# Performance work log

Measured on AMD Instinct MI355X. Metric: run time of the kernel, lower is better.

## Reference

```python
import jax, jax.numpy as jnp
import numpy as np

B = 1024        # batch_size (len(c_ids))
D = 128         # dim_proto
N_AFE_A = 2     # len(AFE_a_ids_selected) == l_a
N_AFE_R = 2     # len(AFE_r_ids_selected) == l_r
S = 16          # sum(n_nbs_per_hop) = 10 + 6
A = 4096        # num_atoms (active codebook rows)
L = N_AFE_A + N_AFE_R * S  # 34


def _normalize(x, eps=1e-12):
    # torch F.normalize(dim=-1): x / max(||x||_2, eps)
    n = jnp.linalg.norm(x, axis=-1, keepdims=True)
    return x / jnp.maximum(n, eps)


def setup_inputs() -> dict:
    key = jax.random.key(0)
    k1, k2, k3 = jax.random.split(key, 3)
    embeddings = jax.random.normal(k1, (B, L, D), dtype=jnp.float32)
    atoms = jax.random.uniform(k2, (A, D), dtype=jnp.float32, minval=0.0, maxval=0.5)
    W_att = jax.random.normal(k3, ((N_AFE_A + N_AFE_R * S) * D, N_AFE_R * S + N_AFE_A), dtype=jnp.float32) * 0.02
    b_att = jnp.zeros((N_AFE_R * S + N_AFE_A,), dtype=jnp.float32)
    return {"embeddings": embeddings, "atoms": atoms, "W_att": W_att, "b_att": b_att}


def reference(embeddings, atoms, W_att, b_att):
    atoms_n = _normalize(atoms)  # F.normalize(self.atoms[0:num_atoms], dim=-1), [A, D]

    # --- attribute emb sets: embeddings[:, i, :] for i in range(n_AFE_a) ---
    attr = embeddings[:, :N_AFE_A, :]                                 # [B, la, D]
    soft_a = jnp.einsum('bld,ad->bla', attr, atoms_n)                 # similarity vs codebook
    hard_a = (soft_a == soft_a.max(axis=-1, keepdims=True)).astype(jnp.float32)
    assoc_a = jnp.einsum('bla,ad->bld', hard_a, atoms)                # one-hot @ atoms (lookup)

    # --- relational emb sets: chunks of size S, flattened to [B*S, D] in torch ---
    rel = embeddings[:, N_AFE_A:, :].reshape(B, N_AFE_R, S, D)
    soft_r = jnp.einsum('brsd,ad->brsa', rel, atoms_n)
    hard_r = (soft_r == soft_r.max(axis=-1, keepdims=True)).astype(jnp.float32)
    assoc_r = jnp.einsum('brsa,ad->brsd', hard_r, atoms).reshape(B, N_AFE_R * S, D)

    # per-row L2 normalize each associated prototype, then concat along slot dim
    assoc = jnp.concatenate([_normalize(assoc_a), _normalize(assoc_r)], axis=1)  # [B, la+lr*S, D]

    # attention aggregation: Linear over flattened slots, then bmm
    a = assoc.reshape(B, (N_AFE_A + N_AFE_R * S) * D)
    att = a @ W_att + b_att                                           # [B, la+lr*S]
    obj_embs = _normalize(jnp.einsum('bl,bld->bd', att, assoc))       # [B, D]
    return obj_embs
```

## Files before the change

kernel.cpp:

```cpp
#include <hip/hip_runtime.h>
#include <math.h>

#define BB 1024
#define LL 34
#define DD 128
#define AA 4096
#define NROWS (BB * LL)
#define RTILES (NROWS / 16)
#define ATILES (AA / 16)
#define NSPLIT 8
#define TPS (ATILES / NSPLIT)
#define TAU 2.5e-3f
#define SCOREBLKS ((RTILES / 16) * NSPLIT)
#define GTABBLKS (LL * 32)

typedef _Float16 f16;
typedef _Float16 f16x8 __attribute__((ext_vector_type(8)));
typedef float f32x4  __attribute__((ext_vector_type(4)));

#define OFF_EMBA   0u
#define OFF_ATOMB  8912896u
#define OFF_WFRAG  9961472u
#define OFF_G      10379264u
#define OFF_PQ     30433280u
#define OFF_INVN64 34889728u
#define OFF_INVNF  34922496u

__global__ __launch_bounds__(256) void k_prep(const float* __restrict__ emb,
                                              const float* __restrict__ atoms,
                                              const float* __restrict__ W,
                                              double* __restrict__ invn64,
                                              float* __restrict__ invnF,
                                              f16x8* __restrict__ embA,
                                              f16x8* __restrict__ atomB,
                                              f16x8* __restrict__ wfrag) {
    __shared__ __align__(16) float stbuf[4608];
    __shared__ double part[16][17];
    const int bid = blockIdx.x;
    const int tid = threadIdx.x;

    if (bid < RTILES + ATILES) {
        const bool isAtom = (bid >= RTILES);
        const int tile = isAtom ? bid - RTILES : bid;
        const float* src = (isAtom ? atoms : emb) + (size_t)tile * 2048;
        float4* st4 = (float4*)stbuf;
        for (int i = tid; i < 512; i += 256) {
            int row = i >> 5, c4 = i & 31;
            st4[row * 33 + c4] = ((const float4*)src)[i];
        }
        __syncthreads();

        const int ks = tid >> 6, l = tid & 63;
        const int m = l & 15, koff4 = ((l >> 4) << 1) + (ks << 3);
        float4 f0 = st4[m * 33 + koff4];
        float4 f1 = st4[m * 33 + koff4 + 1];
        float xs[8] = {f0.x, f0.y, f0.z, f0.w, f1.x, f1.y, f1.z, f1.w};

        if (!isAtom) {
            f16x8 h;
            #pragma unroll
            for (int j = 0; j < 8; j++) h[j] = (f16)xs[j];
            embA[(size_t)(tile * 4 + ks) * 64 + l] = h;
        } else {
            double ssq = 0.0;
            #pragma unroll
            for (int j = 0; j < 8; j++) ssq += (double)xs[j] * xs[j];
            part[m][ks * 4 + (l >> 4)] = ssq;
            __syncthreads();
            double tot = 0.0;
            #pragma unroll
            for (int q = 0; q < 16; q++) tot += part[m][q];
            double n = sqrt(tot);
            if (n < 1e-12) n = 1e-12;
            double inv = 1.0 / n;
            float invf = (float)inv;
            f16x8 h;
            #pragma unroll
            for (int j = 0; j < 8; j++) h[j] = (f16)(xs[j] * invf);
            if (ks == 0 && (l >> 4) == 0) {
                invn64[tile * 16 + m] = inv;
                invnF[tile * 16 + m] = invf;
            }
            atomB[(size_t)(tile * 4 + ks) * 64 + l] = h;
        }
    } else {
        const int l = bid - RTILES - ATILES;
        const float* wsrc = W + (size_t)l * 128 * LL;
        for (int i = tid; i < 128 * LL; i += 256) {
            int row = i / LL, j = i - row * LL;
            stbuf[row * 35 + j] = wsrc[i];
        }
        __syncthreads();
        for (int s = tid; s < 768; s += 256) {
            int lane = s & 63, ksnt = s >> 6;
            int ks = ksnt & 3, nt = ksnt >> 2;
            int j = nt * 16 + (lane & 15);
            int kb = ks * 32 + ((lane >> 4) << 3);
            f16x8 h;
            if (j < LL) {
                #pragma unroll
                for (int jj = 0; jj < 8; jj++) h[jj] = (f16)stbuf[(kb + jj) * 35 + j];
            } else {
                #pragma unroll
                for (int jj = 0; jj < 8; jj++) h[jj] = (f16)0.f;
            }
            wfrag[(size_t)((l * 3 + nt) * 4 + ks) * 64 + lane] = h;
        }
    }
}

__global__ __launch_bounds__(256, 3) void k_score(const f16x8* __restrict__ embA,
                                                  const char* __restrict__ atomB,
                                                  const f16x8* __restrict__ wfrag,
                                                  float* __restrict__ G,
                                                  float4* __restrict__ pq) {
    const int tid = threadIdx.x;
    const int w = tid >> 6, l = tid & 63;

    if (blockIdx.x >= SCOREBLKS) {
        __shared__ __align__(16) float gs[128 * 36];
        const int gb = blockIdx.x - SCOREBLKS;
        const int ll = gb >> 5, ab = gb & 31;

        f16x8 bw[3][4];
        #pragma unroll
        for (int nt = 0; nt < 3; nt++)
            #pragma unroll
            for (int ks = 0; ks < 4; ks++)
                bw[nt][ks] = wfrag[(size_t)((ll * 3 + nt) * 4 + ks) * 64 + l];

        const int col = l & 15, rq = (l >> 4) * 4;
        #pragma unroll
        for (int t = 0; t < 2; t++) {
            int atile = ab * 8 + w * 2 + t;
            f16x8 ah[4];
            #pragma unroll
            for (int ks = 0; ks < 4; ks++)
                ah[ks] = *(const f16x8*)(atomB + ((size_t)(atile * 4 + ks) * 64 + l) * 16);
            f32x4 acc[3];
            #pragma unroll
            for (int nt = 0; nt < 3; nt++) acc[nt] = (f32x4){0.f, 0.f, 0.f, 0.f};
            #pragma unroll
            for (int ks = 0; ks < 4; ks++)
                #pragma unroll
                for (int nt = 0; nt < 3; nt++)
                    acc[nt] = __builtin_amdgcn_mfma_f32_16x16x32_f16(ah[ks], bw[nt][ks], acc[nt], 0, 0, 0);
            int aloc0 = (w * 2 + t) * 16 + rq;
            #pragma unroll
            for (int nt = 0; nt < 3; nt++) {
                int j = nt * 16 + col;
                if (j < LL) {
                    #pragma unroll
                    for (int r = 0; r < 4; r++)
                        gs[(aloc0 + r) * 36 + j] = acc[nt][r];
                }
            }
        }
        __syncthreads();
        float* Gl = G + ((size_t)ll * 4096 + ab * 128) * 36;
        for (int i = tid; i < 128 * 36; i += 256) Gl[i] = gs[i];
        return;
    }

    const int sp = blockIdx.x / 136, rb = blockIdx.x - sp * 136;
    const int rt0 = rb * 16 + w * 4;

    f16x8 a[4][4];
    #pragma unroll
    for (int f = 0; f < 4; f++)
        #pragma unroll
        for (int ks = 0; ks < 4; ks++)
            a[f][ks] = embA[(size_t)((rt0 + f) * 4 + ks) * 64 + l];

    float v1[16], v2[16];
    #pragma unroll
    for (int s = 0; s < 16; s++) { v1[s] = -3e38f; v2[s] = -3e38f; }

    const f16x8* bbase = (const f16x8*)(atomB) + (size_t)sp * TPS * 256;

    #define LOADT(BUF, T)                                            \
        {                                                            \
            _Pragma("unroll")                                        \
            for (int ks = 0; ks < 4; ks++)                           \
                BUF[ks] = bbase[(size_t)(T) * 256 + ks * 64 + l];    \
        }

    #define COMP(BUF, T)                                                          \
        {                                                                         \
            f32x4 acc[4];                                                         \
            _Pragma("unroll")                                                     \
            for (int f = 0; f < 4; f++) acc[f] = (f32x4){0.f, 0.f, 0.f, 0.f};     \
            _Pragma("unroll")                                                     \
            for (int ks = 0; ks < 4; ks++)                                        \
                _Pragma("unroll")                                                 \
                for (int f = 0; f < 4; f++)                                       \
                    acc[f] = __builtin_amdgcn_mfma_f32_16x16x32_f16(a[f][ks], BUF[ks], acc[f], 0, 0, 0); \
            const unsigned tl = (unsigned)(T);                                    \
            _Pragma("unroll")                                                     \
            for (int f = 0; f < 4; f++)                                           \
                _Pragma("unroll")                                                 \
                for (int r = 0; r < 4; r++) {                                     \
                    int s = f * 4 + r;                                            \
                    float xq = __uint_as_float((__float_as_uint(acc[f][r]) & 0xFFFFFFE0u) | tl); \
                    v2[s] = __builtin_amdgcn_fmed3f(xq, v1[s], v2[s]);            \
                    v1[s] = fmaxf(v1[s], xq);                                     \
                }                                                                 \
        }

    f16x8 c0[4], c1[4];
    LOADT(c0, 0);
    for (int t = 0; t < TPS; t += 2) {
        LOADT(c1, t + 1);
        COMP(c0, t);
        if (t + 2 < TPS) LOADT(c0, t + 2);
        COMP(c1, t + 1);
    }
    #undef LOADT
    #undef COMP

    float vv1[16], vv2[16];
    int jj1[16], jj2[16];
    const int col = l & 15;
    #pragma unroll
    for (int s = 0; s < 16; s++) {
        unsigned u1 = __float_as_uint(v1[s]);
        unsigned u2 = __float_as_uint(v2[s]);
        vv1[s] = __uint_as_float(u1 & 0xFFFFFFE0u);
        vv2[s] = __uint_as_float(u2 & 0xFFFFFFE0u);
        jj1[s] = (sp * TPS + (int)(u1 & 31u)) * 16 + col;
        jj2[s] = (sp * TPS + (int)(u2 & 31u)) * 16 + col;
    }

    #pragma unroll
    for (int m = 1; m <= 8; m <<= 1) {
        #pragma unroll
        for (int s = 0; s < 16; s++) {
            float ov1 = __shfl_xor(vv1[s], m);
            float ov2 = __shfl_xor(vv2[s], m);
            int   oi1 = __shfl_xor(jj1[s], m);
            int   oi2 = __shfl_xor(jj2[s], m);
            bool sel = ov1 > vv1[s];
            float lv  = sel ? vv1[s] : ov1;
            int   li  = sel ? jj1[s] : oi1;
            float wv2 = sel ? ov2 : vv2[s];
            int   wi2 = sel ? oi2 : jj2[s];
            vv1[s] = sel ? ov1 : vv1[s];
            jj1[s] = sel ? oi1 : jj1[s];
            bool s2 = lv > wv2;
            vv2[s] = s2 ? lv : wv2;
            jj2[s] = s2 ? li : wi2;
        }
    }

    if ((l & 15) == 0) {
        int q = l >> 4;
        #pragma unroll
        for (int f = 0; f < 4; f++)
            #pragma unroll
            for (int r = 0; r < 4; r++) {
                int s = f * 4 + r;
                int row = (rt0 + f) * 16 + q * 4 + r;
                float4 o;
                o.x = vv1[s];
                o.y = vv2[s];
                o.z = __int_as_float(jj1[s]);
                o.w = __int_as_float(jj2[s]);
                pq[(size_t)row * NSPLIT + sp] = o;
            }
    }
}

__global__ __launch_bounds__(256) void k_epilogue(const float4* __restrict__ pq,
                                                  const float* __restrict__ emb,
                                                  const float* __restrict__ atoms,
                                                  const double* __restrict__ invn64,
                                                  const float* __restrict__ invnF,
                                                  const float* __restrict__ G,
                                                  const float* __restrict__ b_att,
                                                  float* __restrict__ out) {
    __shared__ __align__(16) float assoc[LL * DD];
    __shared__ __align__(16) float4 pqS[LL][NSPLIT];
    __shared__ int   amaxS[LL];
    __shared__ float invS[LL];
    __shared__ float attS[LL];
    __shared__ float wsum[4][40];
    __shared__ float sqw[4];
    __shared__ int   flagCnt;
    __shared__ int   flagRow[LL];

    const int b = blockIdx.x, tid = threadIdx.x;
    const int wid = tid >> 6, lane = tid & 63;

    if (tid == 0) flagCnt = 0;
    for (int i = tid; i < LL * NSPLIT; i += 256)
        pqS[i >> 3][i & 7] = pq[(size_t)(b * LL + (i >> 3)) * NSPLIT + (i & 7)];
    __syncthreads();

    if (tid < LL) {
        float V1 = -3e38f, V2 = -3e38f;
        int I1 = 0;
        #pragma unroll
        for (int sp = 0; sp < NSPLIT; sp++) {
            float4 qv = pqS[tid][sp];
            float a1 = qv.x, a2 = qv.y;
            int   j1 = __float_as_int(qv.z);
            bool sel = a1 > V1;
            float lv  = sel ? V1 : a1;
            float wv2 = sel ? a2 : V2;
            V1 = sel ? a1 : V1;
            I1 = sel ? j1 : I1;
            V2 = fmaxf(lv, wv2);
        }
        amaxS[tid] = I1;
        if (V1 - V2 < TAU) {
            int k = atomicAdd(&flagCnt, 1);
            flagRow[k] = tid;
        }
    }
    __syncthreads();

    const int cnt = flagCnt;
    for (int fi = wid; fi < cnt; fi += 4) {
        int row = flagRow[fi];
        const float2 ev = ((const float2*)(emb + (size_t)(b * LL + row) * DD))[lane];
        double bestS = -1e300;
        int bestI = 0x7fffffff;
        for (int sp = 0; sp < NSPLIT; sp++) {
            float4 qv = pqS[row][sp];
            #pragma unroll
            for (int h = 0; h < 2; h++) {
                int idx = __float_as_int(h ? qv.w : qv.z);
                const float2 av = ((const float2*)(atoms + (size_t)idx * DD))[lane];
                double p = (double)ev.x * av.x + (double)ev.y * av.y;
                #pragma unroll
                for (int m = 1; m <= 32; m <<= 1) p += __shfl_xor(p, m);
                double sc = p * invn64[idx];
                if (sc > bestS || (sc == bestS && idx < bestI)) { bestS = sc; bestI = idx; }
            }
        }
        if (lane == 0) amaxS[row] = bestI;
    }
    __syncthreads();

    if (tid < LL) invS[tid] = invnF[amaxS[tid]];
    if (lane < LL) {
        float ga = 0.f;
        for (int ll = wid; ll < LL; ll += 4)
            ga += G[((size_t)ll * 4096 + amaxS[ll]) * 36 + lane];
        wsum[wid][lane] = ga;
    }
    __syncthreads();

    for (int idx = tid; idx < LL * DD; idx += 256) {
        int ll = idx >> 7, d = idx & 127;
        assoc[idx] = atoms[(size_t)amaxS[ll] * DD + d] * invS[ll];
    }
    if (tid < LL)
        attS[tid] = b_att[tid] + wsum[0][tid] + wsum[1][tid] + wsum[2][tid] + wsum[3][tid];
    __syncthreads();

    float o = 0.0f;
    if (tid < DD) {
        #pragma unroll
        for (int ll = 0; ll < LL; ll++) o = fmaf(attS[ll], assoc[ll * DD + tid], o);
    }
    float sq = (tid < DD) ? o * o : 0.0f;
    #pragma unroll
    for (int off = 32; off; off >>= 1) sq += __shfl_xor(sq, off);
    if (lane == 0) sqw[wid] = sq;
    __syncthreads();
    float tot = sqw[0] + sqw[1] + sqw[2] + sqw[3];
    float n = sqrtf(tot);
    float inv = 1.0f / fmaxf(n, 1e-12f);
    if (tid < DD) out[(size_t)b * DD + tid] = o * inv;
}

extern "C" void kernel_launch(void* const* d_in, const int* in_sizes, int n_in,
                              void* d_out, int out_size, void* d_ws, size_t ws_size,
                              hipStream_t stream) {
    const float* emb   = (const float*)d_in[0];
    const float* atoms = (const float*)d_in[1];
    const float* W     = (const float*)d_in[2];
    const float* b_att = (const float*)d_in[3];
    float* out = (float*)d_out;

    char* ws = (char*)d_ws;
    f16x8*  embA   = (f16x8*)(ws + OFF_EMBA);
    char*   atomB  = (char*)(ws + OFF_ATOMB);
    f16x8*  wfrag  = (f16x8*)(ws + OFF_WFRAG);
    float*  G      = (float*)(ws + OFF_G);
    float4* pq     = (float4*)(ws + OFF_PQ);
    double* invn64 = (double*)(ws + OFF_INVN64);
    float*  invnF  = (float*)(ws + OFF_INVNF);

    k_prep<<<RTILES + ATILES + LL, 256, 0, stream>>>(emb, atoms, W, invn64, invnF,
                                                     embA, (f16x8*)atomB, wfrag);
    k_score<<<SCOREBLKS + GTABBLKS, 256, 0, stream>>>(embA, atomB, wfrag, G, pq);
    k_epilogue<<<BB, 256, 0, stream>>>(pq, emb, atoms, invn64, invnF, G, b_att, out);
}
```

Baseline: 153.5 us.

## Store G table in fp16, deepen atom prefetch, parallelize rescoring, batch prep tiles

The precomputed attention-weight table G is stored as fp16 instead of fp32, which halves its write and gather traffic. The score kernel's atom-tile pipeline goes from double to quad buffering to hide more load latency. The epilogue now spreads the exact fp64 rescoring of ambiguous rows across all 16 candidates per wave, then does a final reduction, instead of scanning them serially per row. The prep kernel handles four tiles per block to cut the block count. The fp16 G values add rounding error to the attention logits, and the extra buffers raise register pressure.

```diff
diff --git a/kernel.cpp b/kernel.cpp
--- a/kernel.cpp
+++ b/kernel.cpp
@@ -13,6 +13,7 @@
 #define TAU 2.5e-3f
 #define SCOREBLKS ((RTILES / 16) * NSPLIT)
 #define GTABBLKS (LL * 32)
+#define PREPEA ((RTILES + ATILES) / 4)
 
 typedef _Float16 f16;
 typedef _Float16 f16x8 __attribute__((ext_vector_type(8)));
@@ -22,9 +23,9 @@
 #define OFF_ATOMB  8912896u
 #define OFF_WFRAG  9961472u
 #define OFF_G      10379264u
-#define OFF_PQ     30433280u
-#define OFF_INVN64 34889728u
-#define OFF_INVNF  34922496u
+#define OFF_PQ     20406272u
+#define OFF_INVN64 24862720u
+#define OFF_INVNF  24895488u
 
 __global__ __launch_bounds__(256) void k_prep(const float* __restrict__ emb,
                                               const float* __restrict__ atoms,
@@ -39,52 +40,57 @@
     const int bid = blockIdx.x;
     const int tid = threadIdx.x;
 
-    if (bid < RTILES + ATILES) {
-        const bool isAtom = (bid >= RTILES);
-        const int tile = isAtom ? bid - RTILES : bid;
-        const float* src = (isAtom ? atoms : emb) + (size_t)tile * 2048;
-        float4* st4 = (float4*)stbuf;
-        for (int i = tid; i < 512; i += 256) {
-            int row = i >> 5, c4 = i & 31;
-            st4[row * 33 + c4] = ((const float4*)src)[i];
-        }
-        __syncthreads();
-
-        const int ks = tid >> 6, l = tid & 63;
-        const int m = l & 15, koff4 = ((l >> 4) << 1) + (ks << 3);
-        float4 f0 = st4[m * 33 + koff4];
-        float4 f1 = st4[m * 33 + koff4 + 1];
-        float xs[8] = {f0.x, f0.y, f0.z, f0.w, f1.x, f1.y, f1.z, f1.w};
-
-        if (!isAtom) {
-            f16x8 h;
-            #pragma unroll
-            for (int j = 0; j < 8; j++) h[j] = (f16)xs[j];
-            embA[(size_t)(tile * 4 + ks) * 64 + l] = h;
-        } else {
-            double ssq = 0.0;
-            #pragma unroll
-            for (int j = 0; j < 8; j++) ssq += (double)xs[j] * xs[j];
-            part[m][ks * 4 + (l >> 4)] = ssq;
+    if (bid < PREPEA) {
+        #pragma unroll 1
+        for (int tt = 0; tt < 4; tt++) {
+            const int gtile = bid * 4 + tt;
+            const bool isAtom = (gtile >= RTILES);
+            const int tile = isAtom ? gtile - RTILES : gtile;
+            const float* src = (isAtom ? atoms : emb) + (size_t)tile * 2048;
+            float4* st4 = (float4*)stbuf;
+            for (int i = tid; i < 512; i += 256) {
+                int row = i >> 5, c4 = i & 31;
+                st4[row * 33 + c4] = ((const float4*)src)[i];
+            }
             __syncthreads();
-            double tot = 0.0;
-            #pragma unroll
-            for (int q = 0; q < 16; q++) tot += part[m][q];
-            double n = sqrt(tot);
-            if (n < 1e-12) n = 1e-12;
-            double inv = 1.0 / n;
-            float invf = (float)inv;
-            f16x8 h;
-            #pragma unroll
-            for (int j = 0; j < 8; j++) h[j] = (f16)(xs[j] * invf);
-            if (ks == 0 && (l >> 4) == 0) {
-                invn64[tile * 16 + m] = inv;
-                invnF[tile * 16 + m] = invf;
+
+            const int ks = tid >> 6, l = tid & 63;
+            const int m = l & 15, koff4 = ((l >> 4) << 1) + (ks << 3);
+            float4 f0 = st4[m * 33 + koff4];
+            float4 f1 = st4[m * 33 + koff4 + 1];
+            float xs[8] = {f0.x, f0.y, f0.z, f0.w, f1.x, f1.y, f1.z, f1.w};
+
+            if (!isAtom) {
+                f16x8 h;
+                #pragma unroll
+                for (int j = 0; j < 8; j++) h[j] = (f16)xs[j];
+                embA[(size_t)(tile * 4 + ks) * 64 + l] = h;
+            } else {
+                double ssq = 0.0;
+                #pragma unroll
+                for (int j = 0; j < 8; j++) ssq += (double)xs[j] * xs[j];
+                part[m][ks * 4 + (l >> 4)] = ssq;
+                __syncthreads();
+                double tot = 0.0;
+                #pragma unroll
+                for (int q = 0; q < 16; q++) tot += part[m][q];
+                double n = sqrt(tot);
+                if (n < 1e-12) n = 1e-12;
+                double inv = 1.0 / n;
+                float invf = (float)inv;
+                f16x8 h;
+                #pragma unroll
+                for (int j = 0; j < 8; j++) h[j] = (f16)(xs[j] * invf);
+                if (ks == 0 && (l >> 4) == 0) {
+                    invn64[tile * 16 + m] = inv;
+                    invnF[tile * 16 + m] = invf;
+                }
+                atomB[(size_t)(tile * 4 + ks) * 64 + l] = h;
             }
-            atomB[(size_t)(tile * 4 + ks) * 64 + l] = h;
+            __syncthreads();
         }
     } else {
-        const int l = bid - RTILES - ATILES;
+        const int l = bid - PREPEA;
         const float* wsrc = W + (size_t)l * 128 * LL;
         for (int i = tid; i < 128 * LL; i += 256) {
             int row = i / LL, j = i - row * LL;
@@ -112,7 +118,7 @@
 __global__ __launch_bounds__(256, 3) void k_score(const f16x8* __restrict__ embA,
                                                   const char* __restrict__ atomB,
                                                   const f16x8* __restrict__ wfrag,
-                                                  float* __restrict__ G,
+                                                  f16* __restrict__ Gh,
                                                   float4* __restrict__ pq) {
     const int tid = threadIdx.x;
     const int w = tid >> 6, l = tid & 63;
@@ -157,8 +163,8 @@
             }
         }
         __syncthreads();
-        float* Gl = G + ((size_t)ll * 4096 + ab * 128) * 36;
-        for (int i = tid; i < 128 * 36; i += 256) Gl[i] = gs[i];
+        f16* Gl = Gh + ((size_t)ll * 4096 + ab * 128) * 36;
+        for (int i = tid; i < 128 * 36; i += 256) Gl[i] = (f16)gs[i];
         return;
     }
 
@@ -207,13 +213,17 @@
                 }                                                                 \
         }
 
-    f16x8 c0[4], c1[4];
-    LOADT(c0, 0);
-    for (int t = 0; t < TPS; t += 2) {
-        LOADT(c1, t + 1);
-        COMP(c0, t);
-        if (t + 2 < TPS) LOADT(c0, t + 2);
-        COMP(c1, t + 1);
+    f16x8 b0[4], b1[4], b2[4], b3[4];
+    LOADT(b0, 0);
+    LOADT(b1, 1);
+    for (int t = 0; t < TPS; t += 4) {
+        LOADT(b2, t + 2);
+        LOADT(b3, t + 3);
+        COMP(b0, t);
+        COMP(b1, t + 1);
+        if (t + 4 < TPS) { LOADT(b0, t + 4); LOADT(b1, t + 5); }
+        COMP(b2, t + 2);
+        COMP(b3, t + 3);
     }
     #undef LOADT
     #undef COMP
@@ -275,11 +285,13 @@
                                                   const float* __restrict__ atoms,
                                                   const double* __restrict__ invn64,
                                                   const float* __restrict__ invnF,
-                                                  const float* __restrict__ G,
+                                                  const f16* __restrict__ Gh,
                                                   const float* __restrict__ b_att,
                                                   float* __restrict__ out) {
     __shared__ __align__(16) float assoc[LL * DD];
     __shared__ __align__(16) float4 pqS[LL][NSPLIT];
+    __shared__ double candV[LL][16];
+    __shared__ int    candI[LL][16];
     __shared__ int   amaxS[LL];
     __shared__ float invS[LL];
     __shared__ float attS[LL];
@@ -320,25 +332,32 @@
     __syncthreads();
 
     const int cnt = flagCnt;
-    for (int fi = wid; fi < cnt; fi += 4) {
+    for (int j = wid; j < cnt * 16; j += 4) {
+        int fi = j >> 4, c = j & 15;
         int row = flagRow[fi];
+        float4 qv = pqS[row][c >> 1];
+        int idx = __float_as_int((c & 1) ? qv.w : qv.z);
         const float2 ev = ((const float2*)(emb + (size_t)(b * LL + row) * DD))[lane];
-        double bestS = -1e300;
-        int bestI = 0x7fffffff;
-        for (int sp = 0; sp < NSPLIT; sp++) {
-            float4 qv = pqS[row][sp];
-            #pragma unroll
-            for (int h = 0; h < 2; h++) {
-                int idx = __float_as_int(h ? qv.w : qv.z);
-                const float2 av = ((const float2*)(atoms + (size_t)idx * DD))[lane];
-                double p = (double)ev.x * av.x + (double)ev.y * av.y;
-                #pragma unroll
-                for (int m = 1; m <= 32; m <<= 1) p += __shfl_xor(p, m);
-                double sc = p * invn64[idx];
-                if (sc > bestS || (sc == bestS && idx < bestI)) { bestS = sc; bestI = idx; }
-            }
-        }
-        if (lane == 0) amaxS[row] = bestI;
+        const float2 av = ((const float2*)(atoms + (size_t)idx * DD))[lane];
+        double p = (double)ev.x * av.x + (double)ev.y * av.y;
+        #pragma unroll
+        for (int m = 1; m <= 32; m <<= 1) p += __shfl_xor(p, m);
+        if (lane == 0) {
+            candV[fi][c] = p * invn64[idx];
+            candI[fi][c] = idx;
+        }
+    }
+    __syncthreads();
+    if (tid < cnt) {
+        double bv = -1e300;
+        int bi = 0x7fffffff;
+        #pragma unroll
+        for (int c = 0; c < 16; c++) {
+            double v = candV[tid][c];
+            int    i = candI[tid][c];
+            if (v > bv || (v == bv && i < bi)) { bv = v; bi = i; }
+        }
+        amaxS[flagRow[tid]] = bi;
     }
     __syncthreads();
 
@@ -346,7 +365,7 @@
     if (lane < LL) {
         float ga = 0.f;
         for (int ll = wid; ll < LL; ll += 4)
-            ga += G[((size_t)ll * 4096 + amaxS[ll]) * 36 + lane];
+            ga += (float)Gh[((size_t)ll * 4096 + amaxS[ll]) * 36 + lane];
         wsum[wid][lane] = ga;
     }
     __syncthreads();
@@ -388,13 +407,13 @@
     f16x8*  embA   = (f16x8*)(ws + OFF_EMBA);
     char*   atomB  = (char*)(ws + OFF_ATOMB);
     f16x8*  wfrag  = (f16x8*)(ws + OFF_WFRAG);
-    float*  G      = (float*)(ws + OFF_G);
+    f16*    Gh     = (f16*)(ws + OFF_G);
     float4* pq     = (float4*)(ws + OFF_PQ);
     double* invn64 = (double*)(ws + OFF_INVN64);
     float*  invnF  = (float*)(ws + OFF_INVNF);
 
-    k_prep<<<RTILES + ATILES + LL, 256, 0, stream>>>(emb, atoms, W, invn64, invnF,
-                                                     embA, (f16x8*)atomB, wfrag);
-    k_score<<<SCOREBLKS + GTABBLKS, 256, 0, stream>>>(embA, atomB, wfrag, G, pq);
-    k_epilogue<<<BB, 256, 0, stream>>>(pq, emb, atoms, invn64, invnF, G, b_att, out);
+    k_prep<<<PREPEA + LL, 256, 0, stream>>>(emb, atoms, W, invn64, invnF,
+                                            embA, (f16x8*)atomB, wfrag);
+    k_score<<<SCOREBLKS + GTABBLKS, 256, 0, stream>>>(embA, atomB, wfrag, Gh, pq);
+    k_epilogue<<<BB, 256, 0, stream>>>(pq, emb, atoms, invn64, invnF, Gh, b_att, out);
 }
```

New measurement: 308.0 us. 2.01x slower.
